# Kernel tuning notes

Hardware: AMD Instinct MI355X
Metric: run time of the kernel (lower is better)

The kernel has to match this reference:

```python
import jax, jax.numpy as jnp
import numpy as np

K = 7
PAD = 3
SIZE = K * K
MAX_STEP = 2
IMG_SIZE = 384
EPS = 1e-5


def _unfold(x, k, pad):
    # x: (n, c, h, w) -> (n, c, k*k, h*w), same layout as F.unfold with stride 1
    n, c, h, w = x.shape
    xp = jnp.pad(x, ((0, 0), (0, 0), (pad, pad), (pad, pad)))
    patches = jnp.stack(
        [xp[:, :, i:i + h, j:j + w] for i in range(k) for j in range(k)], axis=2
    )  # (n, c, k*k, h, w)
    return patches.reshape(n, c, k * k, h * w)


def setup_inputs() -> dict:
    key = jax.random.key(0)
    k1, k2, k3, k4 = jax.random.split(key, 4)
    n, c, h, w = 1, 256, 96, 96
    inputs = {
        "input": jax.random.normal(k1, (n, c, h, w), dtype=jnp.float32),
        "weight": jax.random.uniform(k2, (n, SIZE, h * w), dtype=jnp.float32),
        "conv_w": jax.random.normal(k3, (3, c), dtype=jnp.float32) * 0.05,
        "conv_b": jax.random.normal(k4, (3,), dtype=jnp.float32) * 0.05,
    }
    return inputs


def reference(input, weight, conv_w, conv_b):
    n, c, h, w = input.shape
    wc = weight.shape[1] // SIZE  # 1 -> broadcasts over channels
    wgt = weight.reshape(n, wc, SIZE, h * w)
    # row-normalize per-pixel window weights (sym_norm=False branch)
    norm_weight = wgt / (jnp.sum(wgt, axis=2, keepdims=True) + EPS)
    x = input
    for _ in range(MAX_STEP):
        p = _unfold(x, K, PAD)                  # (n, c, k*k, h*w)
        x = (p * norm_weight).sum(axis=2).reshape(n, c, h, w)
    # 1x1 conv latent_dim -> 3
    x = jnp.einsum("nchw,oc->nohw", x, conv_w) + conv_b[None, :, None, None]
    # bilinear upsample, half-pixel centers (== torch align_corners=False)
    x = jax.image.resize(x, (n, 3, IMG_SIZE, IMG_SIZE), method="bilinear")
    return x
```

## Files before the change

### kernel.cpp

```cpp
#include <hip/hip_runtime.h>

#define HW 9216
#define W 96
#define H 96
#define NC 256
#define NT 49
#define NPAIR 25
#define EPSV 1e-5f

#define TS 16
#define HSZ 22
#define CC 8
#define NZ 32

typedef _Float16 half8 __attribute__((ext_vector_type(8)));
typedef _Float16 half2v __attribute__((ext_vector_type(2)));

__global__ __launch_bounds__(256) void pack_kernel(const float* __restrict__ x,
                                                   const float* __restrict__ w,
                                                   _Float16* __restrict__ xpack,
                                                   half2v* __restrict__ nwh) {
    if (blockIdx.y < 8) {
        const int g = blockIdx.y * 4 + (threadIdx.x >> 6);
        const int px = blockIdx.x * 64 + (threadIdx.x & 63);
        const float* __restrict__ sp = x + (size_t)(g * 8) * HW + px;
        half8 h;
#pragma unroll
        for (int c = 0; c < 8; ++c) h[c] = (_Float16)sp[c * HW];
        *(half8*)(xpack + ((size_t)g * HW + px) * 8) = h;
    } else {
        if (blockIdx.x >= 36) return;
        const int p = blockIdx.x * 256 + threadIdx.x;
        float wv[NT];
        float s = 0.f;
#pragma unroll
        for (int t = 0; t < NT; ++t) { wv[t] = w[t * HW + p]; s += wv[t]; }
        const float inv = 1.f / (s + EPSV);
#pragma unroll
        for (int i = 0; i < NPAIR; ++i) {
            half2v h;
            h[0] = (_Float16)(wv[2 * i] * inv);
            h[1] = (2 * i + 1 < NT) ? (_Float16)(wv[2 * i + 1] * inv) : (_Float16)0.f;
            nwh[i * HW + p] = h;
        }
    }
}

template <int FUSE_CONV>
__global__ __launch_bounds__(256) void step_kernel(const _Float16* __restrict__ xin,
                                                   const half2v* __restrict__ nwh,
                                                   const float* __restrict__ cw,
                                                   void* __restrict__ yout) {
    __shared__ half8 xs[HSZ][HSZ];
    const int tx = threadIdx.x & 15;
    const int ty = threadIdx.x >> 4;
    const int bx = blockIdx.x * TS;
    const int by = blockIdx.y * TS;
    const int px = bx + tx;
    const int py = by + ty;
    const int p = py * W + px;
    const int z = blockIdx.z;

    half2v wu[NPAIR];
#pragma unroll
    for (int i = 0; i < NPAIR; ++i) wu[i] = nwh[i * HW + p];

    const _Float16* __restrict__ xz = xin + (size_t)z * HW * 8;
#pragma unroll
    for (int it = 0; it < 2; ++it) {
        const int i = threadIdx.x + it * 256;
        if (i < HSZ * HSZ) {
            const int hy = i / HSZ;
            const int hx = i - hy * HSZ;
            const int gy = by - 3 + hy;
            const int gx = bx - 3 + hx;
            half8 v;
#pragma unroll
            for (int c = 0; c < 8; ++c) v[c] = (_Float16)0.f;
            if ((unsigned)gy < (unsigned)H && (unsigned)gx < (unsigned)W)
                v = *(const half8*)(xz + (size_t)(gy * W + gx) * 8);
            xs[hy][hx] = v;
        }
    }
    __syncthreads();

    float acc[8];
#pragma unroll
    for (int k = 0; k < 8; ++k) acc[k] = 0.f;

#pragma unroll
    for (int i = 0; i < 7; ++i) {
#pragma unroll
        for (int j = 0; j < 7; ++j) {
            const int t = i * 7 + j;
            const float wf = (float)wu[t >> 1][t & 1];
            const half8 v = xs[ty + i][tx + j];
#pragma unroll
            for (int k = 0; k < 8; ++k)
                acc[k] = fmaf(wf, (float)v[k], acc[k]);
        }
    }

    if (FUSE_CONV) {
        float o0 = 0.f, o1 = 0.f, o2 = 0.f;
        const int cbase = z * CC;
#pragma unroll
        for (int k = 0; k < 8; ++k) {
            const int c = cbase + k;
            o0 = fmaf(acc[k], cw[c], o0);
            o1 = fmaf(acc[k], cw[NC + c], o1);
            o2 = fmaf(acc[k], cw[2 * NC + c], o2);
        }
        float* __restrict__ part = (float*)yout;
        part[(z * 3 + 0) * HW + p] = o0;
        part[(z * 3 + 1) * HW + p] = o1;
        part[(z * 3 + 2) * HW + p] = o2;
    } else {
        half8 h;
#pragma unroll
        for (int k = 0; k < 8; ++k) h[k] = (_Float16)acc[k];
        _Float16* __restrict__ yo = (_Float16*)yout;
        *(half8*)(yo + ((size_t)z * HW + p) * 8) = h;
    }
}

#define OUTS 384
#define SRCP 10
__global__ __launch_bounds__(256) void upsample_kernel(const float* __restrict__ partial,
                                                       const float* __restrict__ cb,
                                                       float* __restrict__ dst) {
    __shared__ float cvs[3][SRCP][SRCP];
    const int X = blockIdx.x * 32;
    const int Y = blockIdx.y * 32;
    const int x0s = X >> 2;
    const int y0s = Y >> 2;

    for (int e = threadIdx.x; e < 3 * SRCP * SRCP; e += 256) {
        int ch = e / (SRCP * SRCP);
        int r = e - ch * (SRCP * SRCP);
        int sy = r / SRCP;
        int sx = r - sy * SRCP;
        int gy = min(max(y0s - 1 + sy, 0), H - 1);
        int gx = min(max(x0s - 1 + sx, 0), W - 1);
        const int p = gy * W + gx;
        float sum = cb[ch];
#pragma unroll
        for (int z = 0; z < NZ; ++z) sum += partial[(z * 3 + ch) * HW + p];
        cvs[ch][sy][sx] = sum;
    }
    __syncthreads();

    const int xl = threadIdx.x & 31;
    const int yl0 = threadIdx.x >> 5;
    const int xo = X + xl;
    const float sxf = xo * 0.25f - 0.375f;
    const float fxf = floorf(sxf);
    const int jx = (int)fxf - (x0s - 1);
    const float fx = sxf - fxf;

#pragma unroll
    for (int k = 0; k < 4; ++k) {
        const int yo = Y + yl0 + 8 * k;
        const float syf = yo * 0.25f - 0.375f;
        const float fyf = floorf(syf);
        const int jy = (int)fyf - (y0s - 1);
        const float fy = syf - fyf;
#pragma unroll
        for (int ch = 0; ch < 3; ++ch) {
            const float v00 = cvs[ch][jy][jx], v01 = cvs[ch][jy][jx + 1];
            const float v10 = cvs[ch][jy + 1][jx], v11 = cvs[ch][jy + 1][jx + 1];
            const float v0 = v00 + (v01 - v00) * fx;
            const float v1 = v10 + (v11 - v10) * fx;
            dst[ch * OUTS * OUTS + yo * OUTS + xo] = v0 + (v1 - v0) * fy;
        }
    }
}

extern "C" void kernel_launch(void* const* d_in, const int* in_sizes, int n_in,
                              void* d_out, int out_size, void* d_ws, size_t ws_size,
                              hipStream_t stream) {
    const float* input  = (const float*)d_in[0];
    const float* weight = (const float*)d_in[1];
    const float* conv_w = (const float*)d_in[2];
    const float* conv_b = (const float*)d_in[3];
    float* out = (float*)d_out;

    char* ws = (char*)d_ws;
    _Float16* xpack = (_Float16*)ws;
    _Float16* x1h   = xpack + (size_t)NZ * HW * 8;
    half2v*   nwh   = (half2v*)(x1h + (size_t)NZ * HW * 8);
    float*  partial = (float*)((char*)nwh + (size_t)NPAIR * HW * 4);

    dim3 gp(144, 9);
    pack_kernel<<<gp, 256, 0, stream>>>(input, weight, xpack, nwh);

    dim3 g(W / TS, H / TS, NZ);
    step_kernel<0><<<g, 256, 0, stream>>>(xpack, nwh, nullptr, (void*)x1h);
    step_kernel<1><<<g, 256, 0, stream>>>(x1h, nwh, conv_w, (void*)partial);

    dim3 gu(OUTS / 32, OUTS / 32);
    upsample_kernel<<<gu, 256, 0, stream>>>(partial, conv_b, out);
}
```

Baseline: 36.01 us.

## Fuse packing and weight normalization into first propagation step kernel

Removes the separate pack kernel. The first step kernel now reads fp32 input directly into its halo tile, converting to fp16 on the way into shared memory. Each block also normalizes the window weights itself in fp32 registers, and only the z==0 blocks write the fp16 normalized weights for the second step. Both step kernels now issue their global halo loads before the weight loads and defer the shared-memory stores, so the memory latencies overlap. The cost is that every one of the 32 channel groups re-reads and re-normalizes the 49 weight planes, and the halo reads are now 8 strided fp32 loads instead of one packed fp16 vector.

```diff
diff --git a/kernel.cpp b/kernel.cpp
--- a/kernel.cpp
+++ b/kernel.cpp
@@ -16,41 +16,10 @@
 typedef _Float16 half8 __attribute__((ext_vector_type(8)));
 typedef _Float16 half2v __attribute__((ext_vector_type(2)));
 
-__global__ __launch_bounds__(256) void pack_kernel(const float* __restrict__ x,
-                                                   const float* __restrict__ w,
-                                                   _Float16* __restrict__ xpack,
-                                                   half2v* __restrict__ nwh) {
-    if (blockIdx.y < 8) {
-        const int g = blockIdx.y * 4 + (threadIdx.x >> 6);
-        const int px = blockIdx.x * 64 + (threadIdx.x & 63);
-        const float* __restrict__ sp = x + (size_t)(g * 8) * HW + px;
-        half8 h;
-#pragma unroll
-        for (int c = 0; c < 8; ++c) h[c] = (_Float16)sp[c * HW];
-        *(half8*)(xpack + ((size_t)g * HW + px) * 8) = h;
-    } else {
-        if (blockIdx.x >= 36) return;
-        const int p = blockIdx.x * 256 + threadIdx.x;
-        float wv[NT];
-        float s = 0.f;
-#pragma unroll
-        for (int t = 0; t < NT; ++t) { wv[t] = w[t * HW + p]; s += wv[t]; }
-        const float inv = 1.f / (s + EPSV);
-#pragma unroll
-        for (int i = 0; i < NPAIR; ++i) {
-            half2v h;
-            h[0] = (_Float16)(wv[2 * i] * inv);
-            h[1] = (2 * i + 1 < NT) ? (_Float16)(wv[2 * i + 1] * inv) : (_Float16)0.f;
-            nwh[i * HW + p] = h;
-        }
-    }
-}
-
-template <int FUSE_CONV>
-__global__ __launch_bounds__(256) void step_kernel(const _Float16* __restrict__ xin,
-                                                   const half2v* __restrict__ nwh,
-                                                   const float* __restrict__ cw,
-                                                   void* __restrict__ yout) {
+__global__ __launch_bounds__(256) void step1_kernel(const float* __restrict__ x,
+                                                    const float* __restrict__ w,
+                                                    _Float16* __restrict__ x1h,
+                                                    half2v* __restrict__ nwh) {
     __shared__ half8 xs[HSZ][HSZ];
     const int tx = threadIdx.x & 15;
     const int ty = threadIdx.x >> 4;
@@ -61,25 +30,126 @@
     const int p = py * W + px;
     const int z = blockIdx.z;
 
-    half2v wu[NPAIR];
-#pragma unroll
-    for (int i = 0; i < NPAIR; ++i) wu[i] = nwh[i * HW + p];
-
-    const _Float16* __restrict__ xz = xin + (size_t)z * HW * 8;
+    const float* __restrict__ xb = x + (size_t)z * CC * HW;
+    float hv[2][8];
+    int hidx[2];
 #pragma unroll
     for (int it = 0; it < 2; ++it) {
         const int i = threadIdx.x + it * 256;
+        hidx[it] = i;
+#pragma unroll
+        for (int c = 0; c < 8; ++c) hv[it][c] = 0.f;
         if (i < HSZ * HSZ) {
             const int hy = i / HSZ;
             const int hx = i - hy * HSZ;
             const int gy = by - 3 + hy;
             const int gx = bx - 3 + hx;
-            half8 v;
-#pragma unroll
-            for (int c = 0; c < 8; ++c) v[c] = (_Float16)0.f;
+            if ((unsigned)gy < (unsigned)H && (unsigned)gx < (unsigned)W) {
+                const float* sp = xb + gy * W + gx;
+#pragma unroll
+                for (int c = 0; c < 8; ++c) hv[it][c] = sp[c * HW];
+            }
+        }
+    }
+
+    float wreg[NT];
+    float s = 0.f;
+#pragma unroll
+    for (int t = 0; t < NT; ++t) { wreg[t] = w[t * HW + p]; s += wreg[t]; }
+    const float inv = 1.f / (s + EPSV);
+#pragma unroll
+    for (int t = 0; t < NT; ++t) wreg[t] *= inv;
+
+    if (z == 0) {
+#pragma unroll
+        for (int i = 0; i < NPAIR; ++i) {
+            half2v h;
+            h[0] = (_Float16)wreg[2 * i];
+            h[1] = (2 * i + 1 < NT) ? (_Float16)wreg[2 * i + 1] : (_Float16)0.f;
+            nwh[i * HW + p] = h;
+        }
+    }
+
+#pragma unroll
+    for (int it = 0; it < 2; ++it) {
+        const int i = hidx[it];
+        if (i < HSZ * HSZ) {
+            const int hy = i / HSZ;
+            const int hx = i - hy * HSZ;
+            half8 h;
+#pragma unroll
+            for (int c = 0; c < 8; ++c) h[c] = (_Float16)hv[it][c];
+            xs[hy][hx] = h;
+        }
+    }
+    __syncthreads();
+
+    float acc[8];
+#pragma unroll
+    for (int k = 0; k < 8; ++k) acc[k] = 0.f;
+
+#pragma unroll
+    for (int i = 0; i < 7; ++i) {
+#pragma unroll
+        for (int j = 0; j < 7; ++j) {
+            const float wf = wreg[i * 7 + j];
+            const half8 v = xs[ty + i][tx + j];
+#pragma unroll
+            for (int k = 0; k < 8; ++k)
+                acc[k] = fmaf(wf, (float)v[k], acc[k]);
+        }
+    }
+
+    half8 h;
+#pragma unroll
+    for (int k = 0; k < 8; ++k) h[k] = (_Float16)acc[k];
+    *(half8*)(x1h + ((size_t)z * HW + p) * 8) = h;
+}
+
+__global__ __launch_bounds__(256) void step2_kernel(const _Float16* __restrict__ xin,
+                                                    const half2v* __restrict__ nwh,
+                                                    const float* __restrict__ cw,
+                                                    float* __restrict__ partial) {
+    __shared__ half8 xs[HSZ][HSZ];
+    const int tx = threadIdx.x & 15;
+    const int ty = threadIdx.x >> 4;
+    const int bx = blockIdx.x * TS;
+    const int by = blockIdx.y * TS;
+    const int px = bx + tx;
+    const int py = by + ty;
+    const int p = py * W + px;
+    const int z = blockIdx.z;
+
+    const _Float16* __restrict__ xz = xin + (size_t)z * HW * 8;
+    half8 hv[2];
+    int hidx[2];
+#pragma unroll
+    for (int it = 0; it < 2; ++it) {
+        const int i = threadIdx.x + it * 256;
+        hidx[it] = i;
+#pragma unroll
+        for (int c = 0; c < 8; ++c) hv[it][c] = (_Float16)0.f;
+        if (i < HSZ * HSZ) {
+            const int hy = i / HSZ;
+            const int hx = i - hy * HSZ;
+            const int gy = by - 3 + hy;
+            const int gx = bx - 3 + hx;
             if ((unsigned)gy < (unsigned)H && (unsigned)gx < (unsigned)W)
-                v = *(const half8*)(xz + (size_t)(gy * W + gx) * 8);
-            xs[hy][hx] = v;
+                hv[it] = *(const half8*)(xz + (size_t)(gy * W + gx) * 8);
+        }
+    }
+
+    half2v wu[NPAIR];
+#pragma unroll
+    for (int i = 0; i < NPAIR; ++i) wu[i] = nwh[i * HW + p];
+
+#pragma unroll
+    for (int it = 0; it < 2; ++it) {
+        const int i = hidx[it];
+        if (i < HSZ * HSZ) {
+            const int hy = i / HSZ;
+            const int hx = i - hy * HSZ;
+            xs[hy][hx] = hv[it];
         }
     }
     __syncthreads();
@@ -101,27 +171,18 @@
         }
     }
 
-    if (FUSE_CONV) {
-        float o0 = 0.f, o1 = 0.f, o2 = 0.f;
-        const int cbase = z * CC;
-#pragma unroll
-        for (int k = 0; k < 8; ++k) {
-            const int c = cbase + k;
-            o0 = fmaf(acc[k], cw[c], o0);
-            o1 = fmaf(acc[k], cw[NC + c], o1);
-            o2 = fmaf(acc[k], cw[2 * NC + c], o2);
-        }
-        float* __restrict__ part = (float*)yout;
-        part[(z * 3 + 0) * HW + p] = o0;
-        part[(z * 3 + 1) * HW + p] = o1;
-        part[(z * 3 + 2) * HW + p] = o2;
-    } else {
-        half8 h;
-#pragma unroll
-        for (int k = 0; k < 8; ++k) h[k] = (_Float16)acc[k];
-        _Float16* __restrict__ yo = (_Float16*)yout;
-        *(half8*)(yo + ((size_t)z * HW + p) * 8) = h;
-    }
+    float o0 = 0.f, o1 = 0.f, o2 = 0.f;
+    const int cbase = z * CC;
+#pragma unroll
+    for (int k = 0; k < 8; ++k) {
+        const int c = cbase + k;
+        o0 = fmaf(acc[k], cw[c], o0);
+        o1 = fmaf(acc[k], cw[NC + c], o1);
+        o2 = fmaf(acc[k], cw[2 * NC + c], o2);
+    }
+    partial[(z * 3 + 0) * HW + p] = o0;
+    partial[(z * 3 + 1) * HW + p] = o1;
+    partial[(z * 3 + 2) * HW + p] = o2;
 }
 
 #define OUTS 384
@@ -186,17 +247,13 @@
     float* out = (float*)d_out;
 
     char* ws = (char*)d_ws;
-    _Float16* xpack = (_Float16*)ws;
-    _Float16* x1h   = xpack + (size_t)NZ * HW * 8;
+    _Float16* x1h   = (_Float16*)ws;
     half2v*   nwh   = (half2v*)(x1h + (size_t)NZ * HW * 8);
     float*  partial = (float*)((char*)nwh + (size_t)NPAIR * HW * 4);
 
-    dim3 gp(144, 9);
-    pack_kernel<<<gp, 256, 0, stream>>>(input, weight, xpack, nwh);
-
     dim3 g(W / TS, H / TS, NZ);
-    step_kernel<0><<<g, 256, 0, stream>>>(xpack, nwh, nullptr, (void*)x1h);
-    step_kernel<1><<<g, 256, 0, stream>>>(x1h, nwh, conv_w, (void*)partial);
+    step1_kernel<<<g, 256, 0, stream>>>(input, weight, x1h, nwh);
+    step2_kernel<<<g, 256, 0, stream>>>(x1h, nwh, conv_w, partial);
 
     dim3 gu(OUTS / 32, OUTS / 32);
     upsample_kernel<<<gu, 256, 0, stream>>>(partial, conv_b, out);
```

Result: faster. 34.75 us (-3.5%).
